# Performance work log

Measured on AMD Instinct MI355X. Metric: run time of the kernel, lower is better.

Reference implementation:

```python
import jax, jax.numpy as jnp
import numpy as np

B, S, D = 4, 2048, 1024


def setup_inputs() -> dict:
    key = jax.random.key(0)
    kq, k1, k2, k3 = jax.random.split(key, 4)
    w_scale = 1.0 / np.sqrt(D)  # ~ glorot scale for square Dense
    q = jax.random.normal(kq, (B, S, D), dtype=jnp.float32)
    Wq = jax.random.normal(k1, (D, D), dtype=jnp.float32) * w_scale
    Wk = jax.random.normal(k2, (D, D), dtype=jnp.float32) * w_scale  # unused in self-attn path (bug in original)
    Wv = jax.random.normal(k3, (D, D), dtype=jnp.float32) * w_scale
    # causal mask: 1 = masked (future), matching tf.where(mask == 1, -1e9, scores)
    mask = jnp.triu(jnp.ones((S, S), dtype=jnp.int32), k=1)
    return {"q": q, "Wq": Wq, "Wk": Wk, "Wv": Wv, "mask": mask}


def reference(q, Wq, Wk, Wv, mask):
    # Self-attention path of the original: k=None, v=None.
    WQ = jnp.einsum('bsd,de->bse', q, Wq)
    # Faithful to the original code: dense_v is applied for BOTH K and V.
    WKV = jnp.einsum('bsd,de->bse', q, Wv)
    d_k = jnp.asarray(D, dtype=q.dtype)
    scores = jnp.einsum('bqd,bkd->bqk', WQ, WKV) / jnp.sqrt(d_k)  # [B,S,S]
    scores = jnp.where(mask == 1, jnp.asarray(-1e9, scores.dtype), scores)
    attn = jax.nn.softmax(scores, axis=-1)
    return jnp.einsum('bqk,bkd->bqd', attn, WKV)
```

## Files before the change

### kernel.cpp

```cpp
#include <hip/hip_runtime.h>


typedef unsigned short u16;
typedef short short8 __attribute__((ext_vector_type(8)));
typedef float floatx4 __attribute__((ext_vector_type(4)));

#define S_LEN 2048
#define D_DIM 1024
#define BK 64

__device__ inline u16 f2b(float f) {
  unsigned u = __float_as_uint(f);
  return (u16)((u + 0x7fffu + ((u >> 16) & 1u)) >> 16);
}

__device__ __forceinline__ void gload16(const u16* g, u16* l) {
  __builtin_amdgcn_global_load_lds(
      (const __attribute__((address_space(1))) void*)g,
      (__attribute__((address_space(3))) void*)l, 16, 0, 0);
}

__global__ __launch_bounds__(256)
void cvt_f32_bf16(const float* __restrict__ src, u16* __restrict__ dst) {
  size_t idx = ((size_t)blockIdx.x * 256 + threadIdx.x) * 8;
  float4 a0 = *(const float4*)&src[idx];
  float4 a1 = *(const float4*)&src[idx + 4];
  short8 v;
  v[0] = (short)f2b(a0.x); v[1] = (short)f2b(a0.y);
  v[2] = (short)f2b(a0.z); v[3] = (short)f2b(a0.w);
  v[4] = (short)f2b(a1.x); v[5] = (short)f2b(a1.y);
  v[6] = (short)f2b(a1.z); v[7] = (short)f2b(a1.w);
  *(short8*)&dst[idx] = v;
}

__global__ __launch_bounds__(256)
void transpose_cvt2(const float* __restrict__ s0, u16* __restrict__ d0_,
                    const float* __restrict__ s1, u16* __restrict__ d1_) {
  __shared__ u16 tile[32][33];
  const float* src = blockIdx.z ? s1 : s0;
  u16* dst = blockIdx.z ? d1_ : d0_;
  int c0 = blockIdx.x * 32, r0 = blockIdx.y * 32;
  int tx = threadIdx.x, ty = threadIdx.y;
  for (int ii = 0; ii < 32; ii += 8)
    tile[ii + ty][tx] = f2b(src[(size_t)(r0 + ii + ty) * 1024 + (c0 + tx)]);
  __syncthreads();
  for (int ii = 0; ii < 32; ii += 8)
    dst[(size_t)(c0 + ii + ty) * 1024 + (r0 + tx)] = tile[tx][ii + ty];
}

__global__ __launch_bounds__(512, 2)
void gemm_proj(const u16* __restrict__ A, const u16* __restrict__ B0,
               const u16* __restrict__ B1, u16* __restrict__ C0,
               u16* __restrict__ C1, u16* __restrict__ WKVt) {
  __shared__ __align__(16) u16 lds[65536];

  int id = blockIdx.x;
  int xcd = id & 7, i5 = id >> 3;
  int m_idx = xcd * 4 + (i5 & 3);
  int n_idx = i5 >> 2;
  int z = n_idx >> 2;
  int n0 = (n_idx & 3) * 256;
  int m0 = m_idx * 256;
  const u16* Bp = z ? B1 : B0;
  u16* Cp = z ? C1 : C0;

  int tid = threadIdx.x;
  int wv = tid >> 6, lane = tid & 63, quad = lane >> 4, l15 = lane & 15;
  int wm = wv >> 2, wn = wv & 3;

  int off_g[2];
#pragma unroll
  for (int l = 0; l < 2; ++l) {
    int chunk = (wv * 2 + l) * 64 + lane;
    int r = chunk >> 3, cs = chunk & 7;
    off_g[l] = r * 1024 + (cs ^ (r & 7)) * 8;
  }
  const u16* As0 = A + (size_t)m0 * 1024;
  const u16* As1 = A + (size_t)(m0 + 128) * 1024;
  const u16* Bs0 = Bp + (size_t)n0 * 1024;
  const u16* Bs1 = Bp + (size_t)(n0 + 128) * 1024;

#define PSTAGE(src, reg)                                                     \
  {                                                                          \
    _Pragma("unroll") for (int l = 0; l < 2; ++l)                            \
        gload16((src) + off_g[l], &lds[(reg) * 8192 + (wv * 2 + l) * 512]);  \
  }

  int aoff[2], boff[2];
#pragma unroll
  for (int kk = 0; kk < 2; ++kk) {
    int c = ((kk * 4 + quad) ^ (l15 & 7)) * 8;
    aoff[kk] = l15 * 64 + c;
    boff[kk] = ((wn & 1) * 64 + l15) * 64 + c;
  }
  const u16* A0p = &lds[(0 + wm) * 8192];
  const u16* A1p = &lds[(4 + wm) * 8192];
  const u16* B0p = &lds[(2 + (wn >> 1)) * 8192];
  const u16* B1p = &lds[(6 + (wn >> 1)) * 8192];

  floatx4 acc[8][4];
#pragma unroll
  for (int i = 0; i < 8; ++i)
#pragma unroll
    for (int j = 0; j < 4; ++j) acc[i][j] = (floatx4){0.f, 0.f, 0.f, 0.f};

#define BARp() __builtin_amdgcn_s_barrier()
#define WLG() asm volatile("s_waitcnt lgkmcnt(0)" ::: "memory")
#define WVM(n) asm volatile("s_waitcnt vmcnt(" #n ")" ::: "memory")

#define RDA(dst, base, fb)                                                 \
  _Pragma("unroll") for (int f = 0; f < 4; ++f)                            \
  _Pragma("unroll") for (int kk = 0; kk < 2; ++kk)                         \
      dst[f][kk] = *(const short8*)&(base)[((fb) + f) * 1024 + aoff[kk]];
#define RDB(dst, base, fb)                                                 \
  _Pragma("unroll") for (int f = 0; f < 2; ++f)                            \
  _Pragma("unroll") for (int kk = 0; kk < 2; ++kk)                         \
      dst[f][kk] = *(const short8*)&(base)[((fb) + f) * 1024 + boff[kk]];
#define MMQ(mh, nh, afq, bfq)                                              \
  __builtin_amdgcn_s_setprio(1);                                           \
  _Pragma("unroll") for (int f = 0; f < 4; ++f)                            \
  _Pragma("unroll") for (int g2 = 0; g2 < 2; ++g2)                         \
  _Pragma("unroll") for (int kk = 0; kk < 2; ++kk)                         \
      acc[(mh) * 4 + f][(nh) * 2 + g2] =                                   \
          __builtin_amdgcn_mfma_f32_16x16x32_bf16(                         \
              afq[f][kk], bfq[g2][kk], acc[(mh) * 4 + f][(nh) * 2 + g2],   \
              0, 0, 0);                                                    \
  __builtin_amdgcn_s_setprio(0);

  PSTAGE(As0, 0); PSTAGE(As1, 1); PSTAGE(Bs0, 2); PSTAGE(Bs1, 3);
  PSTAGE(As0 + 64, 4); PSTAGE(As1 + 64, 5); PSTAGE(Bs0 + 64, 6);
  PSTAGE(Bs1 + 64, 7);
  WVM(8);
  BARp();

#pragma unroll 1
  for (int it = 0; it < 8; ++it) {
    int kb2 = it * 128 + 128, kb3 = it * 128 + 192;
    short8 af[4][2], bf0[2][2], bf1[2][2];
    RDA(af, A0p, 0); RDB(bf0, B0p, 0);
    BARp(); WLG();
    MMQ(0, 0, af, bf0);
    BARp();
    RDB(bf1, B0p, 2);
    BARp(); WLG();
    MMQ(0, 1, af, bf1);
    BARp();
    RDA(af, A0p, 4);
    if (it < 7) PSTAGE(Bs0 + kb2, 2);
    BARp(); WLG();
    MMQ(1, 1, af, bf1);
    BARp();
    if (it < 7) { PSTAGE(Bs1 + kb2, 3); PSTAGE(As0 + kb2, 0); }
    BARp();
    MMQ(1, 0, af, bf0);
    if (it < 7) { WVM(6); } else { WVM(0); }
    BARp();
    RDA(af, A1p, 0); RDB(bf0, B1p, 0);
    if (it < 7) PSTAGE(As1 + kb2, 1);
    BARp(); WLG();
    MMQ(0, 0, af, bf0);
    BARp();
    RDB(bf1, B1p, 2);
    BARp(); WLG();
    MMQ(0, 1, af, bf1);
    BARp();
    RDA(af, A1p, 4);
    if (it < 7) PSTAGE(Bs0 + kb3, 6);
    BARp(); WLG();
    MMQ(1, 1, af, bf1);
    BARp();
    if (it < 7) {
      PSTAGE(Bs1 + kb3, 7); PSTAGE(As0 + kb3, 4); PSTAGE(As1 + kb3, 5);
    }
    BARp();
    MMQ(1, 0, af, bf0);
    if (it < 7) WVM(8);
    BARp();
  }

  asm volatile("s_waitcnt vmcnt(0) lgkmcnt(0)" ::: "memory");
#pragma unroll
  for (int mf = 0; mf < 8; ++mf)
#pragma unroll
    for (int nf = 0; nf < 4; ++nf)
#pragma unroll
      for (int r = 0; r < 4; ++r)
        Cp[(size_t)(m0 + wm * 128 + mf * 16 + quad * 4 + r) * D_DIM +
           (n0 + wn * 64 + nf * 16 + l15)] = f2b(acc[mf][nf][r]);

  if (z) {
    int b = m0 >> 11, srow = m0 & 2047;
    u16* Wt = WKVt + (size_t)b * D_DIM * S_LEN;
#pragma unroll
    for (int ph = 0; ph < 2; ++ph) {
      BARp();
      if ((wn >> 1) == ph) {
#pragma unroll
        for (int mf = 0; mf < 8; ++mf)
#pragma unroll
          for (int nf = 0; nf < 4; ++nf)
#pragma unroll
            for (int r = 0; r < 4; ++r)
              lds[((wn & 1) * 64 + nf * 16 + l15) * 272 +
                  (wm * 128 + mf * 16 + quad * 4 + r)] = f2b(acc[mf][nf][r]);
      }
      BARp();
#pragma unroll
      for (int rr = 0; rr < 8; ++rr) {
        int idx = rr * 512 + tid;
        int dl = idx >> 5, sc = idx & 31;
        *(short8*)&Wt[(size_t)(n0 + ph * 128 + dl) * S_LEN + srow + sc * 8] =
            *(const short8*)&lds[dl * 272 + sc * 8];
      }
    }
  }
}

#define GEMM64_PROLOG()                                                       \
  __shared__ u16 Als[64 * BK];                                                \
  __shared__ u16 Bls[128 * BK];                                               \
  int tid = threadIdx.x;                                                      \
  int wave = tid >> 6, lane = tid & 63, quad = lane >> 4, l15 = lane & 15;    \
  int wr = (wave >> 1) * 32, wc = (wave & 1) * 64;                            \
  int arow = lane >> 3;                                                       \
  int acol = ((lane & 7) ^ (arow & 7)) << 3;                                  \
  floatx4 acc[2][4];                                                          \
  _Pragma("unroll") for (int i = 0; i < 2; ++i)                               \
  _Pragma("unroll") for (int j = 0; j < 4; ++j)                               \
      acc[i][j] = (floatx4){0.f, 0.f, 0.f, 0.f};

#define GEMM64_KLOOP(Aptr, lda, Bptr, ldb, KEND)                              \
  for (int kb = 0; kb < (KEND); kb += BK) {                                   \
    __syncthreads();                                                          \
    _Pragma("unroll") for (int p = 0; p < 2; ++p) {                           \
      int r0 = wave * 16 + p * 8;                                             \
      gload16(&(Aptr)[(size_t)(m0 + r0 + arow) * (lda) + kb + acol],          \
              &Als[r0 * BK]);                                                 \
    }                                                                         \
    _Pragma("unroll") for (int p = 0; p < 4; ++p) {                           \
      int r0 = wave * 32 + p * 8;                                             \
      gload16(&(Bptr)[(size_t)(n0 + r0 + arow) * (ldb) + kb + acol],          \
              &Bls[r0 * BK]);                                                 \
    }                                                                         \
    __syncthreads();                                                          \
    _Pragma("unroll") for (int kk8 = 0; kk8 < 8; kk8 += 4) {                  \
      int cg = (((kk8 + quad) & 7) ^ (l15 & 7)) << 3;                         \
      short8 af[2], bfr[4];                                                   \
      _Pragma("unroll") for (int i = 0; i < 2; ++i)                           \
          af[i] = *(const short8*)&Als[(wr + i * 16 + l15) * BK + cg];        \
      _Pragma("unroll") for (int j = 0; j < 4; ++j)                           \
          bfr[j] = *(const short8*)&Bls[(wc + j * 16 + l15) * BK + cg];       \
      _Pragma("unroll") for (int i = 0; i < 2; ++i)                           \
      _Pragma("unroll") for (int j = 0; j < 4; ++j)                           \
          acc[i][j] = __builtin_amdgcn_mfma_f32_16x16x32_bf16(                \
              af[i], bfr[j], acc[i][j], 0, 0, 0);                             \
    }                                                                         \
  }

__global__ __launch_bounds__(256)
void gemm_scores(const u16* __restrict__ WQ, const u16* __restrict__ WKV,
                 u16* __restrict__ Pp, float* __restrict__ rowsum) {
  int id = blockIdx.x;
  int xcd = id & 7;
  int b = xcd & 3, h = xcd >> 2;
  int t = id >> 3;
  int m = (int)((sqrtf(8.f * (float)t + 1.f) - 1.f) * 0.5f);
  while ((m + 1) * (m + 2) / 2 <= t) ++m;
  while (m * (m + 1) / 2 > t) --m;
  int bj = t - m * (m + 1) / 2;
  int bi = 2 * m + h;
  int m0 = bi * 64, n0 = bj * 128;
  const u16* A = WQ + (size_t)b * S_LEN * D_DIM;
  const u16* Bp = WKV + (size_t)b * S_LEN * D_DIM;
  GEMM64_PROLOG();
  GEMM64_KLOOP(A, D_DIM, Bp, D_DIM, D_DIM);
  u16* Pb = Pp + (size_t)b * S_LEN * S_LEN;
  float part[2][4];
#pragma unroll
  for (int i = 0; i < 2; ++i)
#pragma unroll
    for (int r = 0; r < 4; ++r) part[i][r] = 0.f;
#pragma unroll
  for (int i = 0; i < 2; ++i)
#pragma unroll
    for (int j = 0; j < 4; ++j) {
      int col = n0 + wc + j * 16 + l15;
#pragma unroll
      for (int r = 0; r < 4; ++r) {
        int row = m0 + wr + i * 16 + quad * 4 + r;
        float p = (col > row) ? 0.f : __expf(acc[i][j][r] * 0.03125f);
        Pb[(size_t)row * S_LEN + col] = f2b(p);
        part[i][r] += p;
      }
    }
#pragma unroll
  for (int i = 0; i < 2; ++i)
#pragma unroll
    for (int r = 0; r < 4; ++r) {
      float v = part[i][r];
#pragma unroll
      for (int off = 1; off < 16; off <<= 1) v += __shfl_xor(v, off, 64);
      part[i][r] = v;
    }
  if (l15 == 0) {
#pragma unroll
    for (int i = 0; i < 2; ++i)
#pragma unroll
      for (int r = 0; r < 4; ++r)
        atomicAdd(&rowsum[b * S_LEN + m0 + wr + i * 16 + quad * 4 + r],
                  part[i][r]);
  }
}

__global__ __launch_bounds__(256)
void gemm_pv(const u16* __restrict__ Pp, const u16* __restrict__ WKVt,
             const float* __restrict__ rowsum, float* __restrict__ out) {
  int id = blockIdx.x;
  int xcd = id & 7;
  int b = xcd & 3, h = xcd >> 2;
  int r_ = id >> 3;
  int mh = 15 - (r_ >> 3);
  int bi = 2 * mh + h;
  int bj = r_ & 7;
  int m0 = bi * 64, n0 = bj * 128;
  int kend = (bi + 1) * 64;
  const u16* A = Pp + (size_t)b * S_LEN * S_LEN;
  const u16* Bp = WKVt + (size_t)b * (size_t)D_DIM * S_LEN;
  GEMM64_PROLOG();
  GEMM64_KLOOP(A, S_LEN, Bp, S_LEN, kend);
  const float* rs = rowsum + b * S_LEN;
  float* Co = out + (size_t)b * S_LEN * D_DIM;
#pragma unroll
  for (int i = 0; i < 2; ++i)
#pragma unroll
    for (int r = 0; r < 4; ++r) {
      int row = m0 + wr + i * 16 + quad * 4 + r;
      float inv = 1.0f / rs[row];
#pragma unroll
      for (int j = 0; j < 4; ++j)
        Co[(size_t)row * D_DIM + (n0 + wc + j * 16 + l15)] =
            acc[i][j][r] * inv;
    }
}

extern "C" void kernel_launch(void* const* d_in, const int* in_sizes, int n_in,
                              void* d_out, int out_size, void* d_ws, size_t ws_size,
                              hipStream_t stream) {
  const float* q = (const float*)d_in[0];
  const float* Wq = (const float*)d_in[1];
  const float* Wv = (const float*)d_in[3];
  char* ws = (char*)d_ws;
  const size_t MB = 1024 * 1024;
  u16* Wqt = (u16*)(ws);
  u16* Wvt = (u16*)(ws + 2 * MB);
  u16* qb16 = (u16*)(ws + 4 * MB);
  u16* Pp = (u16*)(ws);
  u16* WQ = (u16*)(ws + 32 * MB);
  u16* WKV = (u16*)(ws + 48 * MB);
  u16* WKVt = (u16*)(ws + 64 * MB);
  float* rowsum = (float*)(ws + 80 * MB);

  hipMemsetAsync(rowsum, 0, 4 * S_LEN * sizeof(float), stream);
  cvt_f32_bf16<<<4096, 256, 0, stream>>>(q, qb16);
  transpose_cvt2<<<dim3(32, 32, 2), dim3(32, 8), 0, stream>>>(Wq, Wqt, Wv, Wvt);
  gemm_proj<<<256, 512, 0, stream>>>(qb16, Wqt, Wvt, WQ, WKV, WKVt);
  gemm_scores<<<1088, 256, 0, stream>>>(WQ, WKV, Pp, rowsum);
  gemm_pv<<<1024, 256, 0, stream>>>(Pp, WKVt, rowsum, (float*)d_out);
}
```

Before: 209.7 us.

## Enlarge attention GEMM tiles to 128x128 and fuse prep kernels into one launch

New measurement: 222.9 us. 1.06x slower.

```diff
diff --git a/kernel.cpp b/kernel.cpp
--- a/kernel.cpp
+++ b/kernel.cpp
@@ -21,31 +21,45 @@
 }
 
 __global__ __launch_bounds__(256)
-void cvt_f32_bf16(const float* __restrict__ src, u16* __restrict__ dst) {
-  size_t idx = ((size_t)blockIdx.x * 256 + threadIdx.x) * 8;
-  float4 a0 = *(const float4*)&src[idx];
-  float4 a1 = *(const float4*)&src[idx + 4];
-  short8 v;
-  v[0] = (short)f2b(a0.x); v[1] = (short)f2b(a0.y);
-  v[2] = (short)f2b(a0.z); v[3] = (short)f2b(a0.w);
-  v[4] = (short)f2b(a1.x); v[5] = (short)f2b(a1.y);
-  v[6] = (short)f2b(a1.z); v[7] = (short)f2b(a1.w);
-  *(short8*)&dst[idx] = v;
-}
-
-__global__ __launch_bounds__(256)
-void transpose_cvt2(const float* __restrict__ s0, u16* __restrict__ d0_,
-                    const float* __restrict__ s1, u16* __restrict__ d1_) {
-  __shared__ u16 tile[32][33];
-  const float* src = blockIdx.z ? s1 : s0;
-  u16* dst = blockIdx.z ? d1_ : d0_;
-  int c0 = blockIdx.x * 32, r0 = blockIdx.y * 32;
-  int tx = threadIdx.x, ty = threadIdx.y;
-  for (int ii = 0; ii < 32; ii += 8)
-    tile[ii + ty][tx] = f2b(src[(size_t)(r0 + ii + ty) * 1024 + (c0 + tx)]);
+void prep(const float* __restrict__ q, u16* __restrict__ qb16,
+          const float* __restrict__ Wq, u16* __restrict__ Wqt,
+          const float* __restrict__ Wv, u16* __restrict__ Wvt,
+          float* __restrict__ rowsum) {
+  int id = blockIdx.x, tid = threadIdx.x;
+  if (id < 4096) {
+    if (id < 4) {
+      int o = id * 2048 + tid * 8;
+      float4 zz = {0.f, 0.f, 0.f, 0.f};
+      *(float4*)&rowsum[o] = zz;
+      *(float4*)&rowsum[o + 4] = zz;
+    }
+    size_t idx = ((size_t)id * 256 + tid) * 8;
+    float4 a0 = *(const float4*)&q[idx];
+    float4 a1 = *(const float4*)&q[idx + 4];
+    short8 v;
+    v[0] = (short)f2b(a0.x); v[1] = (short)f2b(a0.y);
+    v[2] = (short)f2b(a0.z); v[3] = (short)f2b(a0.w);
+    v[4] = (short)f2b(a1.x); v[5] = (short)f2b(a1.y);
+    v[6] = (short)f2b(a1.z); v[7] = (short)f2b(a1.w);
+    *(short8*)&qb16[idx] = v;
+    return;
+  }
+  __shared__ u16 tile[64][65];
+  int id2 = id - 4096;
+  int z = id2 >> 8;
+  int idx4 = id2 & 255;
+  int c0 = (idx4 & 15) * 64, r0 = (idx4 >> 4) * 64;
+  const float* src = z ? Wv : Wq;
+  u16* dst = z ? Wvt : Wqt;
+  int tx = tid & 63, ty = tid >> 6;
+#pragma unroll
+  for (int i = 0; i < 16; ++i)
+    tile[i * 4 + ty][tx] =
+        f2b(src[(size_t)(r0 + i * 4 + ty) * 1024 + (c0 + tx)]);
   __syncthreads();
-  for (int ii = 0; ii < 32; ii += 8)
-    dst[(size_t)(c0 + ii + ty) * 1024 + (r0 + tx)] = tile[tx][ii + ty];
+#pragma unroll
+  for (int i = 0; i < 16; ++i)
+    dst[(size_t)(c0 + i * 4 + ty) * 1024 + (r0 + tx)] = tile[tx][i * 4 + ty];
 }
 
 __global__ __launch_bounds__(512, 2)
@@ -216,44 +230,41 @@
   }
 }
 
-#define GEMM64_PROLOG()                                                       \
-  __shared__ u16 Als[64 * BK];                                                \
-  __shared__ u16 Bls[128 * BK];                                               \
+#define GEMM128_PROLOG()                                                      \
+  __shared__ __align__(16) u16 Als[128 * BK];                                 \
+  __shared__ __align__(16) u16 Bls[128 * BK];                                 \
   int tid = threadIdx.x;                                                      \
   int wave = tid >> 6, lane = tid & 63, quad = lane >> 4, l15 = lane & 15;    \
-  int wr = (wave >> 1) * 32, wc = (wave & 1) * 64;                            \
+  int wm = (wave >> 1) * 64, wn = (wave & 1) * 64;                            \
   int arow = lane >> 3;                                                       \
   int acol = ((lane & 7) ^ (arow & 7)) << 3;                                  \
-  floatx4 acc[2][4];                                                          \
-  _Pragma("unroll") for (int i = 0; i < 2; ++i)                               \
+  floatx4 acc[4][4];                                                          \
+  _Pragma("unroll") for (int ii = 0; ii < 4; ++ii)                            \
   _Pragma("unroll") for (int j = 0; j < 4; ++j)                               \
-      acc[i][j] = (floatx4){0.f, 0.f, 0.f, 0.f};
-
-#define GEMM64_KLOOP(Aptr, lda, Bptr, ldb, KEND)                              \
+      acc[ii][j] = (floatx4){0.f, 0.f, 0.f, 0.f};
+
+#define GEMM128_KLOOP(Aptr, lda, Bptr, ldb, KEND)                             \
   for (int kb = 0; kb < (KEND); kb += BK) {                                   \
     __syncthreads();                                                          \
-    _Pragma("unroll") for (int p = 0; p < 2; ++p) {                           \
-      int r0 = wave * 16 + p * 8;                                             \
+    _Pragma("unroll") for (int p = 0; p < 4; ++p) {                           \
+      int r0 = p * 32 + wave * 8;                                             \
       gload16(&(Aptr)[(size_t)(m0 + r0 + arow) * (lda) + kb + acol],          \
               &Als[r0 * BK]);                                                 \
-    }                                                                         \
-    _Pragma("unroll") for (int p = 0; p < 4; ++p) {                           \
-      int r0 = wave * 32 + p * 8;                                             \
       gload16(&(Bptr)[(size_t)(n0 + r0 + arow) * (ldb) + kb + acol],          \
               &Bls[r0 * BK]);                                                 \
     }                                                                         \
     __syncthreads();                                                          \
     _Pragma("unroll") for (int kk8 = 0; kk8 < 8; kk8 += 4) {                  \
       int cg = (((kk8 + quad) & 7) ^ (l15 & 7)) << 3;                         \
-      short8 af[2], bfr[4];                                                   \
-      _Pragma("unroll") for (int i = 0; i < 2; ++i)                           \
-          af[i] = *(const short8*)&Als[(wr + i * 16 + l15) * BK + cg];        \
+      short8 af[4], bfr[4];                                                   \
+      _Pragma("unroll") for (int ii = 0; ii < 4; ++ii)                        \
+          af[ii] = *(const short8*)&Als[(wm + ii * 16 + l15) * BK + cg];      \
       _Pragma("unroll") for (int j = 0; j < 4; ++j)                           \
-          bfr[j] = *(const short8*)&Bls[(wc + j * 16 + l15) * BK + cg];       \
-      _Pragma("unroll") for (int i = 0; i < 2; ++i)                           \
+          bfr[j] = *(const short8*)&Bls[(wn + j * 16 + l15) * BK + cg];       \
+      _Pragma("unroll") for (int ii = 0; ii < 4; ++ii)                        \
       _Pragma("unroll") for (int j = 0; j < 4; ++j)                           \
-          acc[i][j] = __builtin_amdgcn_mfma_f32_16x16x32_bf16(                \
-              af[i], bfr[j], acc[i][j], 0, 0, 0);                             \
+          acc[ii][j] = __builtin_amdgcn_mfma_f32_16x16x32_bf16(               \
+              af[ii], bfr[j], acc[ii][j], 0, 0, 0);                           \
     }                                                                         \
   }
 
@@ -264,51 +275,60 @@
   int xcd = id & 7;
   int b = xcd & 3, h = xcd >> 2;
   int t = id >> 3;
-  int m = (int)((sqrtf(8.f * (float)t + 1.f) - 1.f) * 0.5f);
-  while ((m + 1) * (m + 2) / 2 <= t) ++m;
-  while (m * (m + 1) / 2 > t) --m;
-  int bj = t - m * (m + 1) / 2;
+  int m, bj;
+  if (h == 0) {
+    if (t >= 64) return;
+    m = (int)sqrtf((float)t);
+    while ((m + 1) * (m + 1) <= t) ++m;
+    while (m * m > t) --m;
+    bj = t - m * m;
+  } else {
+    m = (int)((sqrtf(4.f * (float)t + 1.f) - 1.f) * 0.5f);
+    while ((m + 1) * (m + 1) + (m + 1) <= t) ++m;
+    while (m * m + m > t) --m;
+    bj = t - m * m - m;
+  }
   int bi = 2 * m + h;
-  int m0 = bi * 64, n0 = bj * 128;
+  int m0 = bi * 128, n0 = bj * 128;
   const u16* A = WQ + (size_t)b * S_LEN * D_DIM;
   const u16* Bp = WKV + (size_t)b * S_LEN * D_DIM;
-  GEMM64_PROLOG();
-  GEMM64_KLOOP(A, D_DIM, Bp, D_DIM, D_DIM);
+  GEMM128_PROLOG();
+  GEMM128_KLOOP(A, D_DIM, Bp, D_DIM, D_DIM);
   u16* Pb = Pp + (size_t)b * S_LEN * S_LEN;
-  float part[2][4];
-#pragma unroll
-  for (int i = 0; i < 2; ++i)
-#pragma unroll
-    for (int r = 0; r < 4; ++r) part[i][r] = 0.f;
-#pragma unroll
-  for (int i = 0; i < 2; ++i)
+  float part[4][4];
+#pragma unroll
+  for (int ii = 0; ii < 4; ++ii)
+#pragma unroll
+    for (int r = 0; r < 4; ++r) part[ii][r] = 0.f;
+#pragma unroll
+  for (int ii = 0; ii < 4; ++ii)
 #pragma unroll
     for (int j = 0; j < 4; ++j) {
-      int col = n0 + wc + j * 16 + l15;
+      int col = n0 + wn + j * 16 + l15;
 #pragma unroll
       for (int r = 0; r < 4; ++r) {
-        int row = m0 + wr + i * 16 + quad * 4 + r;
-        float p = (col > row) ? 0.f : __expf(acc[i][j][r] * 0.03125f);
+        int row = m0 + wm + ii * 16 + quad * 4 + r;
+        float p = (col > row) ? 0.f : __expf(acc[ii][j][r] * 0.03125f);
         Pb[(size_t)row * S_LEN + col] = f2b(p);
-        part[i][r] += p;
+        part[ii][r] += p;
       }
     }
 #pragma unroll
-  for (int i = 0; i < 2; ++i)
+  for (int ii = 0; ii < 4; ++ii)
 #pragma unroll
     for (int r = 0; r < 4; ++r) {
-      float v = part[i][r];
+      float v = part[ii][r];
 #pragma unroll
       for (int off = 1; off < 16; off <<= 1) v += __shfl_xor(v, off, 64);
-      part[i][r] = v;
+      part[ii][r] = v;
     }
   if (l15 == 0) {
 #pragma unroll
-    for (int i = 0; i < 2; ++i)
+    for (int ii = 0; ii < 4; ++ii)
 #pragma unroll
       for (int r = 0; r < 4; ++r)
-        atomicAdd(&rowsum[b * S_LEN + m0 + wr + i * 16 + quad * 4 + r],
-                  part[i][r]);
+        atomicAdd(&rowsum[b * S_LEN + m0 + wm + ii * 16 + quad * 4 + r],
+                  part[ii][r]);
   }
 }
 
@@ -319,27 +339,27 @@
   int xcd = id & 7;
   int b = xcd & 3, h = xcd >> 2;
   int r_ = id >> 3;
-  int mh = 15 - (r_ >> 3);
+  int mh = 7 - (r_ >> 3);
   int bi = 2 * mh + h;
   int bj = r_ & 7;
-  int m0 = bi * 64, n0 = bj * 128;
-  int kend = (bi + 1) * 64;
+  int m0 = bi * 128, n0 = bj * 128;
+  int kend = (bi + 1) * 128;
   const u16* A = Pp + (size_t)b * S_LEN * S_LEN;
   const u16* Bp = WKVt + (size_t)b * (size_t)D_DIM * S_LEN;
-  GEMM64_PROLOG();
-  GEMM64_KLOOP(A, S_LEN, Bp, S_LEN, kend);
+  GEMM128_PROLOG();
+  GEMM128_KLOOP(A, S_LEN, Bp, S_LEN, kend);
   const float* rs = rowsum + b * S_LEN;
   float* Co = out + (size_t)b * S_LEN * D_DIM;
 #pragma unroll
-  for (int i = 0; i < 2; ++i)
+  for (int ii = 0; ii < 4; ++ii)
 #pragma unroll
     for (int r = 0; r < 4; ++r) {
-      int row = m0 + wr + i * 16 + quad * 4 + r;
+      int row = m0 + wm + ii * 16 + quad * 4 + r;
       float inv = 1.0f / rs[row];
 #pragma unroll
       for (int j = 0; j < 4; ++j)
-        Co[(size_t)row * D_DIM + (n0 + wc + j * 16 + l15)] =
-            acc[i][j][r] * inv;
+        Co[(size_t)row * D_DIM + (n0 + wn + j * 16 + l15)] =
+            acc[ii][j][r] * inv;
     }
 }
 
@@ -360,10 +380,8 @@
   u16* WKVt = (u16*)(ws + 64 * MB);
   float* rowsum = (float*)(ws + 80 * MB);
 
-  hipMemsetAsync(rowsum, 0, 4 * S_LEN * sizeof(float), stream);
-  cvt_f32_bf16<<<4096, 256, 0, stream>>>(q, qb16);
-  transpose_cvt2<<<dim3(32, 32, 2), dim3(32, 8), 0, stream>>>(Wq, Wqt, Wv, Wvt);
+  prep<<<4608, 256, 0, stream>>>(q, qb16, Wq, Wqt, Wv, Wvt, rowsum);
   gemm_proj<<<256, 512, 0, stream>>>(qb16, Wqt, Wvt, WQ, WKV, WKVt);
-  gemm_scores<<<1088, 256, 0, stream>>>(WQ, WKV, Pp, rowsum);
-  gemm_pv<<<1024, 256, 0, stream>>>(Pp, WKVt, rowsum, (float*)d_out);
-}
+  gemm_scores<<<576, 256, 0, stream>>>(WQ, WKV, Pp, rowsum);
+  gemm_pv<<<512, 256, 0, stream>>>(Pp, WKVt, rowsum, (float*)d_out);
+}
```
